# Optimization experiments

Measured on AMD Instinct MI355X. Metric: run time of the kernel, lower is better.

Reference implementation:

```python
import jax, jax.numpy as jnp
import numpy as np


def setup_inputs() -> dict:
    key = jax.random.key(0)
    attn = jax.random.uniform(key, (64, 1024, 1024), dtype=jnp.float32)
    return {"attn": attn}


def reference(attn) -> jnp.ndarray:
    # attn: [B, N, N]. For each sample, group strictly-upper-triangular
    # elements by diagonal offset k = j - i (k = 1..N-2; the k = N-1
    # diagonal has a single element and is excluded, matching the torch
    # loop `for i in range(len(distance_record) - 1)`).
    # For offset k: std (unbiased, ddof=1) of diag elements scaled by
    # (N-k)/5, i.e. std(x) * (N-k)/5. Then mean over k, then mean over B.
    B, N = attn.shape[0], attn.shape[1]
    ii = jnp.arange(N)
    off = ii[None, :] - ii[:, None]              # [N, N], j - i
    upper = off >= 1                              # strict upper triangle
    seg = jnp.where(upper, off, 0).reshape(-1)    # segment id per element
    m = upper.reshape(-1).astype(attn.dtype)      # mask lower/diag to 0

    x = attn.reshape(B, -1) * m                   # [B, N*N]
    segsum = lambda v: jax.ops.segment_sum(v, seg, num_segments=N)
    s1 = jax.vmap(segsum)(x)                      # [B, N] per-offset sums
    s2 = jax.vmap(segsum)(x * x)                  # [B, N] per-offset sum sq

    n = (N - jnp.arange(N)).astype(attn.dtype)    # count per offset k
    mean = s1 / n
    denom = jnp.maximum(n - 1.0, 1.0)             # ddof=1; guard k=N-1 (excluded)
    var = jnp.maximum(s2 - n * mean * mean, 0.0) / denom
    std = jnp.sqrt(var) * (n / 5.0)               # std of scaled values

    per_sample = jnp.mean(std[:, 1:N - 1], axis=1)  # offsets 1..N-2
    return jnp.mean(per_sample)
```

## Files before the change

kernel.cpp:

```cpp
#include <hip/hip_runtime.h>


#define NN 1024
#define NB 64
#define WSTRIDE 1032

template<int RCH>
__global__ __launch_bounds__(256) void diag_pass1(
    const float* __restrict__ attn, float* __restrict__ ws) {
  const int b = blockIdx.x / RCH;
  const int c = blockIdx.x % RCH;
  const int t = threadIdx.x;
  int p = (4 - (c & 3)) & 3; if (p == 0) p = 4;

  const float* __restrict__ base = attn + ((size_t)b << 20);
  const int k0 = p + 4 * t;

  float s1x = 0.f, s1y = 0.f, s1z = 0.f, s1w = 0.f;
  float s2x = 0.f, s2y = 0.f, s2z = 0.f, s2w = 0.f;
  float e1 = 0.f, e2 = 0.f;
  const int ek = t - 248;

  #pragma unroll 4
  for (int i = c; i < NN; i += RCH) {
    const int lim = NN - i;
    const float* __restrict__ rowd = base + (size_t)i * (NN + 1);
    if (k0 < lim) {
      const float4 v = *reinterpret_cast<const float4*>(rowd + k0);
      const float x0 = v.x;
      const float x1 = (k0 + 1 < lim) ? v.y : 0.f;
      const float x2 = (k0 + 2 < lim) ? v.z : 0.f;
      const float x3 = (k0 + 3 < lim) ? v.w : 0.f;
      s1x += x0; s2x += x0 * x0;
      s1y += x1; s2y += x1 * x1;
      s1z += x2; s2z += x2 * x2;
      s1w += x3; s2w += x3 * x3;
    }
    if (ek >= 1 && ek < p && ek < lim) {
      const float x = rowd[ek];
      e1 += x; e2 += x * x;
    }
  }

  float* __restrict__ w1 = ws + (size_t)blockIdx.x * (2 * WSTRIDE);
  float* __restrict__ w2 = w1 + WSTRIDE;
  *reinterpret_cast<float4*>(w1 + 4 * t) = make_float4(s1x, s1y, s1z, s1w);
  *reinterpret_cast<float4*>(w2 + 4 * t) = make_float4(s2x, s2y, s2z, s2w);
  if (ek >= 1 && ek < p) {
    w1[1024 + ek] = e1;
    w2[1024 + ek] = e2;
  }
}

template<int RCH>
__global__ __launch_bounds__(256) void diag_pass2(
    const float* __restrict__ ws, float* __restrict__ part) {
  const int b  = blockIdx.x >> 4;
  const int kg = blockIdx.x & 15;
  const int t  = threadIdx.x;
  const int kk = t & 63;
  const int cg = t >> 6;
  const int k  = kg * 64 + kk;

  int p = (4 - cg) & 3; if (p == 0) p = 4;
  const int idx = (k >= p) ? (k - p) : (1024 + k);

  float s1 = 0.f, s2 = 0.f;
  #pragma unroll
  for (int c = cg; c < RCH; c += 4) {
    const float* __restrict__ w1 = ws + (size_t)(b * RCH + c) * (2 * WSTRIDE);
    s1 += w1[idx];
    s2 += w1[WSTRIDE + idx];
  }

  __shared__ float r1[256], r2[256];
  r1[t] = s1; r2[t] = s2;
  __syncthreads();
  if (t < 128) { r1[t] += r1[t + 128]; r2[t] += r2[t + 128]; }
  __syncthreads();
  if (t < 64) {
    s1 = r1[t] + r1[t + 64];
    s2 = r2[t] + r2[t + 64];
    float acc = 0.f;
    if (k >= 1 && k <= NN - 2) {
      const float n = (float)(NN - k);
      const float mean = s1 / n;
      const float var = fmaxf(s2 - n * mean * mean, 0.f) / (n - 1.f);
      acc = sqrtf(var) * (n * 0.2f);
    }
    #pragma unroll
    for (int s = 32; s > 0; s >>= 1) acc += __shfl_down(acc, s);
    if (t == 0) part[blockIdx.x] = acc;
  }
}

__global__ __launch_bounds__(256) void diag_pass3(
    const float* __restrict__ part, float* __restrict__ out) {
  const int t = threadIdx.x;
  float v = part[t] + part[t + 256] + part[t + 512] + part[t + 768];
  __shared__ float red[256];
  red[t] = v;
  __syncthreads();
  #pragma unroll
  for (int s = 128; s > 0; s >>= 1) {
    if (t < s) red[t] += red[t + s];
    __syncthreads();
  }
  if (t == 0) out[0] = red[0] * (1.0f / (1022.0f * 64.0f));
}

template<int RCH>
static void launch_all(const float* attn, float* out, float* ws,
                       hipStream_t stream) {
  float* part = ws + (size_t)NB * RCH * 2 * WSTRIDE;
  diag_pass1<RCH><<<NB * RCH, 256, 0, stream>>>(attn, ws);
  diag_pass2<RCH><<<NB * 16, 256, 0, stream>>>(ws, part);
  diag_pass3<<<1, 256, 0, stream>>>(part, out);
}

extern "C" void kernel_launch(void* const* d_in, const int* in_sizes, int n_in,
                              void* d_out, int out_size, void* d_ws, size_t ws_size,
                              hipStream_t stream) {
  const float* attn = (const float*)d_in[0];
  float* out = (float*)d_out;
  float* ws = (float*)d_ws;

  const size_t need16 = ((size_t)NB * 16 * 2 * WSTRIDE + 1024) * 4;
  const size_t need8  = ((size_t)NB * 8  * 2 * WSTRIDE + 1024) * 4;

  if (ws_size >= need16)      launch_all<16>(attn, out, ws, stream);
  else if (ws_size >= need8)  launch_all<8>(attn, out, ws, stream);
  else                        launch_all<4>(attn, out, ws, stream);
}
```

Before: 43.97 us.

## Balance triangular diagonal workload by pairing mirrored column groups per thread

Each thread now handles two column groups, its own and the mirrored one, splitting their row ranges so every thread does similar work on the triangular region. Exact trip counts replace per-iteration bounds checks. Edge diagonal elements are reduced with wave shuffles instead of in the main loop. Workspace doubles and the smaller-workspace fallbacks are removed, which risks failure if the workspace is too small.

```diff
diff --git a/kernel.cpp b/kernel.cpp
--- a/kernel.cpp
+++ b/kernel.cpp
@@ -3,56 +3,86 @@
 
 #define NN 1024
 #define NB 64
-#define WSTRIDE 1032
+#define RCH 16
+#define W 1032
 
-template<int RCH>
 __global__ __launch_bounds__(256) void diag_pass1(
     const float* __restrict__ attn, float* __restrict__ ws) {
-  const int b = blockIdx.x / RCH;
-  const int c = blockIdx.x % RCH;
+  const int b = blockIdx.x >> 4;
+  const int c = blockIdx.x & 15;
   const int t = threadIdx.x;
   int p = (4 - (c & 3)) & 3; if (p == 0) p = 4;
 
   const float* __restrict__ base = attn + ((size_t)b << 20);
-  const int k0 = p + 4 * t;
+  const float* __restrict__ rowc = base + (size_t)c * (NN + 1);
+  const size_t stride = (size_t)RCH * (NN + 1);
 
-  float s1x = 0.f, s1y = 0.f, s1z = 0.f, s1w = 0.f;
-  float s2x = 0.f, s2y = 0.f, s2z = 0.f, s2w = 0.f;
-  float e1 = 0.f, e2 = 0.f;
-  const int ek = t - 248;
+  const int k0a = p + 4 * t;
+  const int dfA = 1020 - c - p - 4 * t;
+  const int TfA = (dfA >= 0) ? ((dfA >> 4) + 1) : 0;
+  const int SaA = (TfA + 1) >> 1;
 
-  #pragma unroll 4
-  for (int i = c; i < NN; i += RCH) {
-    const int lim = NN - i;
-    const float* __restrict__ rowd = base + (size_t)i * (NN + 1);
-    if (k0 < lim) {
-      const float4 v = *reinterpret_cast<const float4*>(rowd + k0);
-      const float x0 = v.x;
-      const float x1 = (k0 + 1 < lim) ? v.y : 0.f;
-      const float x2 = (k0 + 2 < lim) ? v.z : 0.f;
-      const float x3 = (k0 + 3 < lim) ? v.w : 0.f;
-      s1x += x0; s2x += x0 * x0;
-      s1y += x1; s2y += x1 * x1;
-      s1z += x2; s2z += x2 * x2;
-      s1w += x3; s2w += x3 * x3;
-    }
-    if (ek >= 1 && ek < p && ek < lim) {
-      const float x = rowd[ek];
-      e1 += x; e2 += x * x;
+  float a1x=0.f,a1y=0.f,a1z=0.f,a1w=0.f,a2x=0.f,a2y=0.f,a2z=0.f,a2w=0.f;
+  {
+    const float* ptr = rowc + k0a;
+    #pragma unroll 4
+    for (int m = 0; m < SaA; ++m) {
+      const float4 v = *reinterpret_cast<const float4*>(ptr + (size_t)m * stride);
+      a1x += v.x; a2x += v.x * v.x;
+      a1y += v.y; a2y += v.y * v.y;
+      a1z += v.z; a2z += v.z * v.z;
+      a1w += v.w; a2w += v.w * v.w;
     }
   }
 
-  float* __restrict__ w1 = ws + (size_t)blockIdx.x * (2 * WSTRIDE);
-  float* __restrict__ w2 = w1 + WSTRIDE;
-  *reinterpret_cast<float4*>(w1 + 4 * t) = make_float4(s1x, s1y, s1z, s1w);
-  *reinterpret_cast<float4*>(w2 + 4 * t) = make_float4(s2x, s2y, s2z, s2w);
-  if (ek >= 1 && ek < p) {
-    w1[1024 + ek] = e1;
-    w2[1024 + ek] = e2;
+  const int qB  = 255 - t;
+  const int k0b = p + 4 * qB;
+  const int dfB = 4 * t - c - p;
+  const int TfB = (dfB >= 0) ? ((dfB >> 4) + 1) : 0;
+  const int SaB = (TfB + 1) >> 1;
+
+  float b1x=0.f,b1y=0.f,b1z=0.f,b1w=0.f,b2x=0.f,b2y=0.f,b2z=0.f,b2w=0.f;
+  {
+    const float* ptr = rowc + k0b;
+    #pragma unroll 4
+    for (int m = SaB; m < TfB; ++m) {
+      const float4 v = *reinterpret_cast<const float4*>(ptr + (size_t)m * stride);
+      b1x += v.x; b2x += v.x * v.x;
+      b1y += v.y; b2y += v.y * v.y;
+      b1z += v.z; b2z += v.z * v.z;
+      b1w += v.w; b2w += v.w * v.w;
+    }
+  }
+
+  float* __restrict__ wsA1 = ws + (size_t)blockIdx.x * (4 * W);
+  float* __restrict__ wsB1 = wsA1 + W;
+  float* __restrict__ wsA2 = wsA1 + 2 * W;
+  float* __restrict__ wsB2 = wsA1 + 3 * W;
+
+  *reinterpret_cast<float4*>(wsA1 + 4 * t)  = make_float4(a1x,a1y,a1z,a1w);
+  *reinterpret_cast<float4*>(wsA2 + 4 * t)  = make_float4(a2x,a2y,a2z,a2w);
+  *reinterpret_cast<float4*>(wsB1 + 4 * qB) = make_float4(b1x,b1y,b1z,b1w);
+  *reinterpret_cast<float4*>(wsB2 + 4 * qB) = make_float4(b2x,b2y,b2z,b2w);
+
+  const int e = t >> 6;
+  if (e >= 1 && e < p) {
+    const int l = t & 63;
+    const int i = c + RCH * l;
+    float x = 0.f;
+    if (i + e < NN) x = base[(size_t)i * (NN + 1) + e];
+    float e1 = x, e2 = x * x;
+    #pragma unroll
+    for (int s = 1; s < 64; s <<= 1) {
+      e1 += __shfl_xor(e1, s);
+      e2 += __shfl_xor(e2, s);
+    }
+    if (l == 0) {
+      wsA1[1024 + e] = e1;  wsA2[1024 + e] = e2;
+      wsB1[1024 + e] = 0.f; wsB2[1024 + e] = 0.f;
+    }
   }
 }
 
-template<int RCH>
 __global__ __launch_bounds__(256) void diag_pass2(
     const float* __restrict__ ws, float* __restrict__ part) {
   const int b  = blockIdx.x >> 4;
@@ -68,9 +98,9 @@
   float s1 = 0.f, s2 = 0.f;
   #pragma unroll
   for (int c = cg; c < RCH; c += 4) {
-    const float* __restrict__ w1 = ws + (size_t)(b * RCH + c) * (2 * WSTRIDE);
-    s1 += w1[idx];
-    s2 += w1[WSTRIDE + idx];
+    const float* __restrict__ w0 = ws + (size_t)(b * RCH + c) * (4 * W);
+    s1 += w0[idx] + w0[W + idx];
+    s2 += w0[2 * W + idx] + w0[3 * W + idx];
   }
 
   __shared__ float r1[256], r2[256];
@@ -109,15 +139,6 @@
   if (t == 0) out[0] = red[0] * (1.0f / (1022.0f * 64.0f));
 }
 
-template<int RCH>
-static void launch_all(const float* attn, float* out, float* ws,
-                       hipStream_t stream) {
-  float* part = ws + (size_t)NB * RCH * 2 * WSTRIDE;
-  diag_pass1<RCH><<<NB * RCH, 256, 0, stream>>>(attn, ws);
-  diag_pass2<RCH><<<NB * 16, 256, 0, stream>>>(ws, part);
-  diag_pass3<<<1, 256, 0, stream>>>(part, out);
-}
-
 extern "C" void kernel_launch(void* const* d_in, const int* in_sizes, int n_in,
                               void* d_out, int out_size, void* d_ws, size_t ws_size,
                               hipStream_t stream) {
@@ -125,10 +146,9 @@
   float* out = (float*)d_out;
   float* ws = (float*)d_ws;
 
-  const size_t need16 = ((size_t)NB * 16 * 2 * WSTRIDE + 1024) * 4;
-  const size_t need8  = ((size_t)NB * 8  * 2 * WSTRIDE + 1024) * 4;
+  float* part = ws + (size_t)NB * RCH * 4 * W;
 
-  if (ws_size >= need16)      launch_all<16>(attn, out, ws, stream);
-  else if (ws_size >= need8)  launch_all<8>(attn, out, ws, stream);
-  else                        launch_all<4>(attn, out, ws, stream);
+  diag_pass1<<<NB * RCH, 256, 0, stream>>>(attn, ws);
+  diag_pass2<<<NB * 16, 256, 0, stream>>>(ws, part);
+  diag_pass3<<<1, 256, 0, stream>>>(part, out);
 }
```

After: 40.90 us. 1.07x faster.

## Balance pass1 work by pairing top and bottom row blocks per workgroup

Applied to the files above, without the earlier changes.

Pass1 now gives each of 32 workgroups per sample a 16-row chunk from the top of the matrix and a mirrored 16-row chunk from the bottom, so every workgroup reads a similar number of upper-triangle elements. Alignment-phase bins are kept in registers and merged through shared memory into per-offset sums, so pass2 indexes by offset directly without phase remapping. Wavefronts whose whole column range is past the row length skip their loads. This adds shared-memory traffic, a barrier and more workspace, and it drops the fallback for smaller workspace sizes.

```diff
diff --git a/kernel.cpp b/kernel.cpp
--- a/kernel.cpp
+++ b/kernel.cpp
@@ -3,56 +3,115 @@
 
 #define NN 1024
 #define NB 64
-#define WSTRIDE 1032
+#define GPS 32
+#define WP 1032
+#define CW (2 * WP)
 
-template<int RCH>
 __global__ __launch_bounds__(256) void diag_pass1(
     const float* __restrict__ attn, float* __restrict__ ws) {
-  const int b = blockIdx.x / RCH;
-  const int c = blockIdx.x % RCH;
+  const int bid = blockIdx.x;
+  const int b = bid >> 5;
+  const int g = bid & 31;
   const int t = threadIdx.x;
-  int p = (4 - (c & 3)) & 3; if (p == 0) p = 4;
+  const int w = t >> 6;
 
   const float* __restrict__ base = attn + ((size_t)b << 20);
-  const int k0 = p + 4 * t;
+  const int i0t = 16 * g;
+  const int i0b = 1008 - 16 * g;
 
-  float s1x = 0.f, s1y = 0.f, s1z = 0.f, s1w = 0.f;
-  float s2x = 0.f, s2y = 0.f, s2z = 0.f, s2w = 0.f;
-  float e1 = 0.f, e2 = 0.f;
-  const int ek = t - 248;
+  float bin1[7] = {0.f,0.f,0.f,0.f,0.f,0.f,0.f};
+  float bin2[7] = {0.f,0.f,0.f,0.f,0.f,0.f,0.f};
 
-  #pragma unroll 4
-  for (int i = c; i < NN; i += RCH) {
-    const int lim = NN - i;
-    const float* __restrict__ rowd = base + (size_t)i * (NN + 1);
-    if (k0 < lim) {
-      const float4 v = *reinterpret_cast<const float4*>(rowd + k0);
-      const float x0 = v.x;
-      const float x1 = (k0 + 1 < lim) ? v.y : 0.f;
-      const float x2 = (k0 + 2 < lim) ? v.z : 0.f;
-      const float x3 = (k0 + 3 < lim) ? v.w : 0.f;
-      s1x += x0; s2x += x0 * x0;
-      s1y += x1; s2y += x1 * x1;
-      s1z += x2; s2z += x2 * x2;
-      s1w += x3; s2w += x3 * x3;
+  if (256 * w < 1024 - 16 * g) {
+    #pragma unroll
+    for (int r = 0; r < 16; ++r) {
+      const int p = 4 - (r & 3);
+      const int s = p + 4 * t;
+      const int L = 1024 - (i0t + r);
+      if (s < L) {
+        const float4 v = *reinterpret_cast<const float4*>(
+            base + (size_t)(i0t + r) * (NN + 1) + s);
+        bin1[p - 1] += v.x; bin2[p - 1] += v.x * v.x;
+        bin1[p    ] += v.y; bin2[p    ] += v.y * v.y;
+        bin1[p + 1] += v.z; bin2[p + 1] += v.z * v.z;
+        bin1[p + 2] += v.w; bin2[p + 2] += v.w * v.w;
+      }
     }
-    if (ek >= 1 && ek < p && ek < lim) {
-      const float x = rowd[ek];
-      e1 += x; e2 += x * x;
+  }
+  if (256 * w < 16 * g + 16) {
+    #pragma unroll
+    for (int r = 0; r < 16; ++r) {
+      const int p = 4 - (r & 3);
+      const int s = p + 4 * t;
+      const int L = 1024 - (i0b + r);
+      if (s < L) {
+        const float4 v = *reinterpret_cast<const float4*>(
+            base + (size_t)(i0b + r) * (NN + 1) + s);
+        bin1[p - 1] += v.x; bin2[p - 1] += v.x * v.x;
+        bin1[p    ] += v.y; bin2[p    ] += v.y * v.y;
+        bin1[p + 1] += v.z; bin2[p + 1] += v.z * v.z;
+        bin1[p + 2] += v.w; bin2[p + 2] += v.w * v.w;
+      }
     }
   }
 
-  float* __restrict__ w1 = ws + (size_t)blockIdx.x * (2 * WSTRIDE);
-  float* __restrict__ w2 = w1 + WSTRIDE;
-  *reinterpret_cast<float4*>(w1 + 4 * t) = make_float4(s1x, s1y, s1z, s1w);
-  *reinterpret_cast<float4*>(w2 + 4 * t) = make_float4(s2x, s2y, s2z, s2w);
-  if (ek >= 1 && ek < p) {
-    w1[1024 + ek] = e1;
-    w2[1024 + ek] = e2;
+  __shared__ float L1[7 * 256], L2[7 * 256];
+  __shared__ float E1[4], E2[4];
+  #pragma unroll
+  for (int bq = 0; bq < 7; ++bq) {
+    L1[bq * 256 + t] = bin1[bq];
+    L2[bq * 256 + t] = bin2[bq];
+  }
+
+  if (w == 3) {
+    const int l = t & 63;
+    float x = 0.f; int e = 0;
+    if (l < 48) {
+      const int h = l / 24, m = l % 24;
+      const int grp = m / 6, idx = m % 6;
+      const int dr = idx < 3 ? 0 : (idx < 5 ? 1 : 2);
+      const int ee = idx < 3 ? idx + 1 : (idx < 5 ? idx - 2 : 1);
+      const int i = (h ? i0b : i0t) + grp * 4 + dr;
+      if (ee < 1024 - i) {
+        x = base[(size_t)i * (NN + 1) + ee];
+        e = ee;
+      }
+    }
+    const float xx = x * x;
+    #pragma unroll
+    for (int eb = 1; eb <= 3; ++eb) {
+      float v1 = (e == eb) ? x : 0.f;
+      float v2 = (e == eb) ? xx : 0.f;
+      #pragma unroll
+      for (int sft = 1; sft < 64; sft <<= 1) {
+        v1 += __shfl_xor(v1, sft);
+        v2 += __shfl_xor(v2, sft);
+      }
+      if (l == 0) { E1[eb] = v1; E2[eb] = v2; }
+    }
+  }
+  __syncthreads();
+
+  float* __restrict__ wout = ws + (size_t)bid * CW;
+  #pragma unroll
+  for (int j = 0; j < 4; ++j) {
+    const int k = 1 + t + 256 * j;
+    if (k <= 1023) {
+      const int b0  = (k - 1) & 3;
+      const int tt0 = (k - 1) >> 2;
+      float s1 = L1[b0 * 256 + tt0];
+      float s2 = L2[b0 * 256 + tt0];
+      if (b0 <= 2 && tt0 >= 1) {
+        s1 += L1[(b0 + 4) * 256 + tt0 - 1];
+        s2 += L2[(b0 + 4) * 256 + tt0 - 1];
+      }
+      if (k <= 3) { s1 += E1[k]; s2 += E2[k]; }
+      wout[k]      = s1;
+      wout[WP + k] = s2;
+    }
   }
 }
 
-template<int RCH>
 __global__ __launch_bounds__(256) void diag_pass2(
     const float* __restrict__ ws, float* __restrict__ part) {
   const int b  = blockIdx.x >> 4;
@@ -62,15 +121,12 @@
   const int cg = t >> 6;
   const int k  = kg * 64 + kk;
 
-  int p = (4 - cg) & 3; if (p == 0) p = 4;
-  const int idx = (k >= p) ? (k - p) : (1024 + k);
-
   float s1 = 0.f, s2 = 0.f;
   #pragma unroll
-  for (int c = cg; c < RCH; c += 4) {
-    const float* __restrict__ w1 = ws + (size_t)(b * RCH + c) * (2 * WSTRIDE);
-    s1 += w1[idx];
-    s2 += w1[WSTRIDE + idx];
+  for (int c = cg; c < GPS; c += 4) {
+    const float* __restrict__ w0 = ws + (size_t)(b * GPS + c) * CW;
+    s1 += w0[k];
+    s2 += w0[WP + k];
   }
 
   __shared__ float r1[256], r2[256];
@@ -109,15 +165,6 @@
   if (t == 0) out[0] = red[0] * (1.0f / (1022.0f * 64.0f));
 }
 
-template<int RCH>
-static void launch_all(const float* attn, float* out, float* ws,
-                       hipStream_t stream) {
-  float* part = ws + (size_t)NB * RCH * 2 * WSTRIDE;
-  diag_pass1<RCH><<<NB * RCH, 256, 0, stream>>>(attn, ws);
-  diag_pass2<RCH><<<NB * 16, 256, 0, stream>>>(ws, part);
-  diag_pass3<<<1, 256, 0, stream>>>(part, out);
-}
-
 extern "C" void kernel_launch(void* const* d_in, const int* in_sizes, int n_in,
                               void* d_out, int out_size, void* d_ws, size_t ws_size,
                               hipStream_t stream) {
@@ -125,10 +172,9 @@
   float* out = (float*)d_out;
   float* ws = (float*)d_ws;
 
-  const size_t need16 = ((size_t)NB * 16 * 2 * WSTRIDE + 1024) * 4;
-  const size_t need8  = ((size_t)NB * 8  * 2 * WSTRIDE + 1024) * 4;
+  float* part = ws + (size_t)NB * GPS * CW;
 
-  if (ws_size >= need16)      launch_all<16>(attn, out, ws, stream);
-  else if (ws_size >= need8)  launch_all<8>(attn, out, ws, stream);
-  else                        launch_all<4>(attn, out, ws, stream);
+  diag_pass1<<<NB * GPS, 256, 0, stream>>>(attn, ws);
+  diag_pass2<<<NB * 16, 256, 0, stream>>>(ws, part);
+  diag_pass3<<<1, 256, 0, stream>>>(part, out);
 }
```

After: 46.20 us. +5.1%, slower.
